# Kernel optimization log

Hardware: AMD Instinct MI355X
Metric: run time of the kernel (lower is better)

The kernel has to match this reference:

```python
import jax, jax.numpy as jnp
import numpy as np

N_HEAD = 16


def _rope_tables(T, head_dim, dtype):
    # RotaryEmbedding buffers: freqs = outer(t, inv_freq), half-dim tables [T, head_dim//2]
    inv_freq = 1.0 / (10000.0 ** (jnp.arange(0, head_dim, 2, dtype=jnp.float32) / head_dim))
    freqs = jnp.arange(T, dtype=jnp.float32)[:, None] * inv_freq[None, :]
    return jnp.cos(freqs).astype(dtype), jnp.sin(freqs).astype(dtype)


def _apply_rotary(x, cos, sin):
    # x: [B,H,T,D]; cos/sin: [T,D//2] broadcast over B,H
    d = x.shape[-1] // 2
    x1, x2 = x[..., :d], x[..., d:]
    return jnp.concatenate([x1 * cos - x2 * sin, x2 * cos + x1 * sin], axis=-1)


def setup_inputs() -> dict:
    key = jax.random.key(0)
    k1, k2, k3 = jax.random.split(key, 3)
    B, T, C = 2, 2048, 2048
    x = jax.random.normal(k1, (B, T, C), dtype=jnp.float32)
    Wqkv = jax.random.normal(k2, (C, 3 * C), dtype=jnp.float32) * (1.0 / np.sqrt(C))
    Wproj = jax.random.normal(k3, (C, C), dtype=jnp.float32) * (1.0 / np.sqrt(C))
    return {"x": x, "Wqkv": Wqkv, "Wproj": Wproj}


def reference(x, Wqkv, Wproj):
    B, T, C = x.shape
    H = N_HEAD
    D = C // H
    qkv = (x @ Wqkv).reshape(B, T, 3, H, D)
    q, k, v = qkv[:, :, 0], qkv[:, :, 1], qkv[:, :, 2]  # [B,T,H,D]
    q = jnp.transpose(q, (0, 2, 1, 3))  # [B,H,T,D]
    k = jnp.transpose(k, (0, 2, 1, 3))
    v = jnp.transpose(v, (0, 2, 1, 3))
    cos, sin = _rope_tables(T, D, x.dtype)
    q = _apply_rotary(q, cos, sin)
    k = _apply_rotary(k, cos, sin)
    scale = 1.0 / np.sqrt(D)
    scores = jnp.einsum('bhqd,bhkd->bhqk', q, k) * scale
    causal = jnp.tril(jnp.ones((T, T), dtype=bool))
    scores = jnp.where(causal, scores, jnp.finfo(scores.dtype).min)
    attn = jax.nn.softmax(scores, axis=-1)
    out = jnp.einsum('bhqk,bhkd->bhqd', attn, v)
    out = jnp.transpose(out, (0, 2, 1, 3)).reshape(B, T, C)
    return out @ Wproj
```

## Files before the change

kernel.cpp:

```cpp
#include <hip/hip_runtime.h>
#include <hip/hip_bf16.h>

typedef short s16b;
using bf16x4 = __attribute__((ext_vector_type(4))) short;
using bf16x8 = __attribute__((ext_vector_type(8))) short;
using f32x4  = __attribute__((ext_vector_type(4))) float;
using u32x4  = __attribute__((ext_vector_type(4))) unsigned;

#define DEVINL __device__ __forceinline__

DEVINL float bf2f(short u) {
    union { float f; unsigned u; } x;
    x.u = ((unsigned)(unsigned short)u) << 16;
    return x.f;
}
DEVINL short f2bf(float f) {
    unsigned u = __builtin_bit_cast(unsigned, f);
    u += 0x7FFFu + ((u >> 16) & 1u);
    return (short)(u >> 16);
}
DEVINL unsigned cvtpk(float a, float b) {
    unsigned r;
    asm("v_cvt_pk_bf16_f32 %0, %1, %2" : "=v"(r) : "v"(a), "v"(b));
    return r;
}

DEVINL f32x4 mfma16(bf16x8 a, bf16x8 b, f32x4 c) {
    return __builtin_amdgcn_mfma_f32_16x16x32_bf16(a, b, c, 0, 0, 0);
}

DEVINL void gload_lds16(const void* g, void* lds_uniform) {
    __builtin_amdgcn_global_load_lds(
        (const __attribute__((address_space(1))) char*)(const char*)g,
        (__attribute__((address_space(3))) char*)(char*)lds_uniform, 16, 0, 0);
}

DEVINL int perm32(int k) {
    return ((k >> 2) & 3) * 8 + ((k >> 4) & 1) * 4 + (k & 3);
}

DEVINL bf16x8 lds128(const s16b* base, int row, int ks, int g) {
    const char* p = (const char*)base + row * 128 + ((((ks << 2) + g) ^ (row & 7)) << 4);
    return *(const bf16x8*)p;
}
DEVINL bf16x8 lds256(const s16b* base, int row, int ds, int g) {
    const char* p = (const char*)base + row * 256 + ((((ds << 2) + g) ^ (row & 7)) << 4);
    return *(const bf16x8*)p;
}

__global__ void k_pre(const float* __restrict__ x, s16b* __restrict__ xb,
                      float* __restrict__ ctab, float* __restrict__ stab) {
    int bid = blockIdx.x;
    if (bid < 512) {
        int idx = bid * 256 + threadIdx.x;
        int i = idx & 63, t = idx >> 6;
        float inv = powf(10000.0f, -(float)i * (1.0f / 64.0f));
        float fr = (float)t * inv;
        ctab[idx] = cosf(fr);
        stab[idx] = sinf(fr);
    } else {
        int idx = (bid - 512) * 256 + threadIdx.x;
        int p = idx * 4;
        int row = p >> 11, pc = p & 2047;
        int grp = pc >> 5, sp = pc & 31;
        int c = sp >> 3, half = (sp >> 2) & 1;
        int ksrc = grp * 32 + half * 16 + c * 4;
        float4 v = *(const float4*)(x + (size_t)row * 2048 + ksrc);
        bf16x4 o;
        o[0] = f2bf(v.x); o[1] = f2bf(v.y); o[2] = f2bf(v.z); o[3] = f2bf(v.w);
        *(bf16x4*)(xb + (size_t)row * 2048 + pc) = o;
    }
}

__global__ void k_tcvt2(const float* __restrict__ Wqkv, s16b* __restrict__ wqkvt,
                        const float* __restrict__ Wproj, s16b* __restrict__ wprojt) {
    __shared__ float tile[32][33];
    int bx = blockIdx.x;
    const float* in; s16b* out; int C, c0;
    if (bx < 192) { in = Wqkv; out = wqkvt; C = 6144; c0 = bx * 32; }
    else          { in = Wproj; out = wprojt; C = 2048; c0 = (bx - 192) * 32; }
    int tx = threadIdx.x & 31, ty = threadIdx.x >> 5;
    int r0 = blockIdx.y * 32;
#pragma unroll
    for (int kk = 0; kk < 4; ++kk) {
        int r = ty + kk * 8;
        tile[r][tx] = in[(size_t)(r0 + r) * C + c0 + tx];
    }
    __syncthreads();
#pragma unroll
    for (int kk = 0; kk < 4; ++kk) {
        int r = ty + kk * 8;
        out[(size_t)(c0 + r) * 2048 + r0 + perm32(tx)] = f2bf(tile[tx][r]);
    }
}

#define STG_B01(DB, KB)                                                        \
  gload_lds16(srcB + (KB), lds + 49152 + (DB) * 32768 + tid16);                \
  gload_lds16(srcB + 262144 + (KB), lds + 49152 + (DB) * 32768 + 8192 + tid16);
#define STG_B23(DB, KB)                                                        \
  gload_lds16(srcB + 524288 + (KB), lds + 49152 + (DB) * 32768 + 16384 + tid16); \
  gload_lds16(srcB + 786432 + (KB), lds + 49152 + (DB) * 32768 + 24576 + tid16);
#define STG_A01(DB, KB)                                                        \
  gload_lds16(srcA + (KB), lds + (DB) * 16384 + tid16);                        \
  gload_lds16(srcA + 262144 + (KB), lds + (DB) * 16384 + 8192 + tid16);

#define AF_READ(B, KS)                                                         \
    _Pragma("unroll")                                                          \
    for (int fi = 0; fi < 4; ++fi) {                                           \
      int row = (fi >> 1) * 64 + wm * 32 + (fi & 1) * 16 + r15;                \
      af[fi] = *(const bf16x8*)(lds + (B) * 16384 + row * 128                  \
               + ((((KS) * 4 + g) ^ (row & 7)) << 4));                         \
    }

#define PH4(B, KH, JH, STGC, WN)                                               \
  {                                                                            \
    if ((JH) == 0) { AF_READ(B, KH) }                                          \
    _Pragma("unroll")                                                          \
    for (int fj = 0; fj < 2; ++fj) {                                           \
      int row = (JH) * 128 + wn * 32 + fj * 16 + r15;                          \
      bfr[fj] = *(const bf16x8*)(lds + 49152 + (B) * 32768 + row * 128         \
                + ((((KH) * 4 + g) ^ (row & 7)) << 4));                        \
    }                                                                          \
    STGC                                                                       \
    if ((WN) == 6) { asm volatile("s_waitcnt vmcnt(6)" ::: "memory");          \
                     __builtin_amdgcn_sched_barrier(0); }                      \
    else if ((WN) == 0) { asm volatile("s_waitcnt vmcnt(0)" ::: "memory");     \
                     __builtin_amdgcn_sched_barrier(0); }                      \
    __builtin_amdgcn_s_barrier();                                              \
    asm volatile("s_waitcnt lgkmcnt(0)" ::: "memory");                         \
    __builtin_amdgcn_sched_barrier(0);                                         \
    __builtin_amdgcn_s_setprio(1);                                             \
    _Pragma("unroll")                                                          \
    for (int fi = 0; fi < 4; ++fi)                                             \
      _Pragma("unroll")                                                        \
      for (int fj = 0; fj < 2; ++fj)                                           \
        acc[fi][(JH) * 2 + fj] = mfma16(af[fi], bfr[fj], acc[fi][(JH) * 2 + fj]); \
    __builtin_amdgcn_s_setprio(0);                                             \
    __builtin_amdgcn_s_barrier();                                              \
    __builtin_amdgcn_sched_barrier(0);                                         \
  }

#define DO_TILE3(B, S1, S2, S3, WNL)                                           \
    PH4(B, 0, 0, S1, -1)                                                       \
    PH4(B, 0, 1, S2, -1)                                                       \
    PH4(B, 1, 0, S3, -1)                                                       \
    PH4(B, 1, 1, , WNL)

#define GEMM3_MAINLOOP(A_, B_)                                                 \
    __shared__ __attribute__((aligned(16))) char lds[147456];                  \
    const int tid = threadIdx.x;                                               \
    const int lane = tid & 63, wave = tid >> 6;                                \
    const int g = lane >> 4, r15 = lane & 15;                                  \
    const int wm = wave >> 2, wn = wave & 3;                                   \
    const int tid16 = tid << 4;                                                \
    const int rowL = tid16 >> 7;                                               \
    const int swzL = ((((tid16 >> 4) & 7) ^ (rowL & 7)) << 4);                 \
    const char* srcA = (const char*)(A_) + (size_t)(bm + rowL) * 4096 + swzL;  \
    const char* srcB = (const char*)(B_) + (size_t)(bn + rowL) * 4096 + swzL;  \
    f32x4 acc[4][4] = {};                                                      \
    bf16x8 af[4], bfr[2];                                                      \
    STG_B01(0, 0) STG_A01(0, 0) STG_B23(0, 0)                                  \
    STG_B01(1, 128) STG_A01(1, 128) STG_B23(1, 128)                            \
    asm volatile("s_waitcnt vmcnt(6)" ::: "memory");                           \
    __builtin_amdgcn_sched_barrier(0);                                         \
    __builtin_amdgcn_s_barrier();                                              \
    for (int t3 = 0; t3 < 10; ++t3) {                                          \
        const int kb2 = (3 * t3 + 2) * 128;                                    \
        const int kb3 = kb2 + 128, kb4 = kb2 + 256;                            \
        DO_TILE3(0, STG_B01(2, kb2), STG_A01(2, kb2), STG_B23(2, kb2), 6)      \
        DO_TILE3(1, STG_B01(0, kb3), STG_A01(0, kb3), STG_B23(0, kb3), 6)      \
        DO_TILE3(2, STG_B01(1, kb4), STG_A01(1, kb4), STG_B23(1, kb4), 6)      \
    }                                                                          \
    DO_TILE3(0, , , , 0)                                                       \
    DO_TILE3(1, , , , -1)

__global__ __launch_bounds__(512) void k_gemm_qkv(
    const s16b* __restrict__ A, const s16b* __restrict__ Bt,
    s16b* __restrict__ Qb, s16b* __restrict__ Kp, s16b* __restrict__ Vt,
    const float* __restrict__ ctab, const float* __restrict__ stab) {
    const int bid = blockIdx.x;
    const int xcd = bid & 7, local = bid >> 3;
    const int rr_ = local >> 5, w = local & 31;
    const int bm = ((xcd & 3) * 8 + (w >> 2)) * 128;
    const int bn = ((xcd >> 2) * 12 + rr_ * 4 + (w & 3)) * 256;
    GEMM3_MAINLOOP(A, Bt)
    const int which = bn >> 11;
    if (which < 2) {
        char* sml = (char*)lds;
#pragma unroll
        for (int i = 0; i < 4; ++i) {
#pragma unroll
            for (int j = 0; j < 4; ++j) {
                int mb0 = (i >> 1) * 64 + wm * 32 + (i & 1) * 16 + 4 * g;
                int nn = (j >> 1) * 128 + wn * 32 + (j & 1) * 16 + r15;
#pragma unroll
                for (int e = 0; e < 4; ++e) {
                    int mm = mb0 + e;
                    *(s16b*)(sml + mm * 528 + ((nn * 2) ^ ((mm & 3) << 5))) =
                        f2bf(acc[i][j][e]);
                }
            }
        }
        __syncthreads();
        const int mrow = tid >> 2, c4 = tid & 3;
        const int bb = bm >> 11;
        const int tt = (bm & 2047) + mrow;
        const char* srow = sml + mrow * 528;
        const int sw = (mrow & 3) << 5;
        bf16x8 v[8];
#pragma unroll
        for (int k = 0; k < 8; ++k) {
            int lc = c4 + 4 * k;
            v[k] = *(const bf16x8*)(srow + ((lc * 16) ^ sw));
        }
        float cs[2][8], sn[2][8];
#pragma unroll
        for (int j = 0; j < 2; ++j) {
            int d0 = 8 * c4 + 32 * j;
            const float* cp = ctab + tt * 64 + d0;
            const float* sp = stab + tt * 64 + d0;
            *(float4*)&cs[j][0] = *(const float4*)cp;
            *(float4*)&cs[j][4] = *(const float4*)(cp + 4);
            *(float4*)&sn[j][0] = *(const float4*)sp;
            *(float4*)&sn[j][4] = *(const float4*)(sp + 4);
        }
        if (which == 0) {
            const float SC = 0.12751744154f;
#pragma unroll
            for (int j = 0; j < 2; ++j)
#pragma unroll
                for (int e = 0; e < 8; ++e) { cs[j][e] *= SC; sn[j][e] *= SC; }
        }
        bf16x8 o[8];
#pragma unroll
        for (int hh = 0; hh < 2; ++hh)
#pragma unroll
            for (int j = 0; j < 2; ++j) {
                int kl = hh * 4 + j, kh = kl + 2;
                bf16x8 r1, r2;
#pragma unroll
                for (int e = 0; e < 8; ++e) {
                    float c = cs[j][e], s = sn[j][e];
                    float x1 = bf2f(v[kl][e]), x2 = bf2f(v[kh][e]);
                    r1[e] = f2bf(x1 * c - x2 * s);
                    r2[e] = f2bf(x2 * c + x1 * s);
                }
                o[kl] = r1; o[kh] = r2;
            }
        if (which == 0) {
#pragma unroll
            for (int k = 0; k < 8; ++k) {
                int lc = c4 + 4 * k;
                int ng = bn + lc * 8;
                int h = (ng >> 7) & 15, d = ng & 127;
                *(bf16x8*)(Qb + ((size_t)(bb * 16 + h) * 2048 + tt) * 128 + d) = o[k];
            }
        } else {
#pragma unroll
            for (int k = 0; k < 8; ++k) {
                int lc = c4 + 4 * k;
                int ng = bn + lc * 8;
                int h = (ng >> 7) & 15, d = ng & 127;
                size_t base = ((size_t)(bb * 16 + h) * 2048 + tt) * 128 + (d & ~31);
                int w2 = d & 31;
                bf16x4 lo, hi;
#pragma unroll
                for (int e = 0; e < 4; ++e) { lo[e] = o[k][e]; hi[e] = o[k][e + 4]; }
                *(bf16x4*)(Kp + base + perm32(w2)) = lo;
                *(bf16x4*)(Kp + base + perm32(w2 + 4)) = hi;
            }
        }
    } else {
#pragma unroll
        for (int i = 0; i < 4; ++i) {
            int m0 = bm + (i >> 1) * 64 + wm * 32 + (i & 1) * 16 + 4 * g;
            int b = m0 >> 11, t0 = m0 & 2047;
            int pt = (t0 & ~31) + perm32(t0 & 31);
#pragma unroll
            for (int j = 0; j < 4; ++j) {
                int n = bn + (j >> 1) * 128 + wn * 32 + (j & 1) * 16 + r15;
                int h = (n >> 7) & 15, d = n & 127;
                size_t base = ((size_t)(b * 16 + h) * 128 + d) * 2048 + pt;
                bf16x4 pk;
#pragma unroll
                for (int e = 0; e < 4; ++e) pk[e] = f2bf(acc[i][j][e]);
                *(bf16x4*)(Vt + base) = pk;
            }
        }
    }
}

__global__ __launch_bounds__(512) void k_gemm_proj(
    const s16b* __restrict__ A, const s16b* __restrict__ Bt, float* __restrict__ Co) {
    const int bid = blockIdx.x;
    const int xcd = bid & 7, local = bid >> 3;
    const int bm = (xcd * 4 + (local & 3)) * 128;
    const int bn = (local >> 2) * 256;
    GEMM3_MAINLOOP(A, Bt)
#pragma unroll
    for (int i = 0; i < 4; ++i) {
        int m0 = bm + (i >> 1) * 64 + wm * 32 + (i & 1) * 16 + 4 * g;
#pragma unroll
        for (int j = 0; j < 4; ++j) {
            int n = bn + (j >> 1) * 128 + wn * 32 + (j & 1) * 16 + r15;
#pragma unroll
            for (int e = 0; e < 4; ++e) Co[(size_t)(m0 + e) * 2048 + n] = acc[i][j][e];
        }
    }
}

__global__ __launch_bounds__(512) void k_attn(
    const s16b* __restrict__ Qb, const s16b* __restrict__ Kp,
    const s16b* __restrict__ Vt, s16b* __restrict__ AO) {
    __shared__ alignas(16) s16b Ks[2][64 * 128];
    __shared__ alignas(16) s16b Vs[2][128 * 64];
    const int tid = threadIdx.x;
    const int lane = tid & 63, wave = tid >> 6;
    const int g = lane >> 4, r15 = lane & 15;
    const int bh = blockIdx.x, pp = blockIdx.y;
    const s16b* Qg = Qb + (size_t)bh * 2048 * 128;
    const char* Kg = (const char*)(Kp + (size_t)bh * 2048 * 128);
    const char* Vg = (const char*)(Vt + (size_t)bh * 128 * 2048);
    const int b = bh >> 4, h = bh & 15;

#define ASTG(BUF, KT)                                                          \
    {                                                                          \
      const int k0s = (KT) * 64;                                               \
      _Pragma("unroll")                                                        \
      for (int rr = 0; rr < 2; ++rr) {                                         \
        int uo = (rr * 512 + wave * 64) * 16;                                  \
        int o = uo + lane * 16;                                                \
        {                                                                      \
          int row = o >> 8, sl = (o >> 4) & 15;                                \
          int sg = (sl ^ (row & 7)) << 4;                                      \
          gload_lds16(Kg + (size_t)(k0s + row) * 256 + sg,                     \
                      (char*)Ks + (BUF) * 16384 + uo);                         \
        }                                                                      \
        {                                                                      \
          int row = o >> 7, sl = (o >> 4) & 7;                                 \
          int sg = (sl ^ (row & 7)) << 4;                                      \
          gload_lds16(Vg + (size_t)row * 4096 + (size_t)k0s * 2 + sg,          \
                      (char*)Vs + (BUF) * 16384 + uo);                         \
        }                                                                      \
      }                                                                        \
    }

    for (int pass = 0; pass < 2; ++pass) {
        const int qt = pass ? pp : (15 - pp);
        const int q0 = qt * 128 + wave * 16;
        const int ktiles = qt * 2 + 2;

        ASTG(0, 0)

        bf16x8 qf[4];
#pragma unroll
        for (int ds = 0; ds < 4; ++ds) {
            const s16b* p = Qg + (size_t)(q0 + r15) * 128 + ds * 32 + 4 * g;
            bf16x4 lo = *(const bf16x4*)p;
            bf16x4 hi = *(const bf16x4*)(p + 16);
            qf[ds] = __builtin_shufflevector(lo, hi, 0, 1, 2, 3, 4, 5, 6, 7);
        }

        f32x4 ot[8] = {};
        float m_s = -3e38f;
        float l_s = 0.f;

        for (int kt = 0; kt < ktiles; ++kt) {
            const int k0 = kt * 64;
            if (kt + 1 < ktiles) {
                ASTG((kt + 1) & 1, kt + 1)
                asm volatile("s_waitcnt vmcnt(4)" ::: "memory");
            } else {
                asm volatile("s_waitcnt vmcnt(0)" ::: "memory");
            }
            __builtin_amdgcn_sched_barrier(0);
            __builtin_amdgcn_s_barrier();
            asm volatile("" ::: "memory");
            __builtin_amdgcn_sched_barrier(0);

            if (k0 <= q0 + 15) {
                const s16b* Kb_ = (const s16b*)((const char*)Ks + (kt & 1) * 16384);
                const s16b* Vb_ = (const s16b*)((const char*)Vs + (kt & 1) * 16384);
                f32x4 st[4] = {};
                __builtin_amdgcn_s_setprio(1);
#pragma unroll
                for (int ds = 0; ds < 4; ++ds) {
#pragma unroll
                    for (int ks = 0; ks < 4; ++ks) {
                        bf16x8 kf = lds256(Kb_, ks * 16 + r15, ds, g);
                        st[ks] = mfma16(kf, qf[ds], st[ks]);
                    }
                }
                __builtin_amdgcn_s_setprio(0);
                if (k0 + 63 > q0) {
#pragma unroll
                    for (int ks = 0; ks < 4; ++ks)
#pragma unroll
                        for (int e = 0; e < 4; ++e) {
                            int kk = k0 + ks * 16 + 4 * g + e;
                            int qq = q0 + r15;
                            if (kk > qq) st[ks][e] = -3e38f;
                        }
                }
                {
                    float mx = st[0][0];
#pragma unroll
                    for (int ks = 0; ks < 4; ++ks)
#pragma unroll
                        for (int e = 0; e < 4; ++e)
                            if (ks | e) mx = fmaxf(mx, st[ks][e]);
                    mx = fmaxf(mx, __shfl_xor(mx, 16));
                    mx = fmaxf(mx, __shfl_xor(mx, 32));
                    if (__any(mx > m_s + 8.f)) {
                        float mn = fmaxf(m_s, mx);
                        float sf = exp2f(m_s - mn);
                        m_s = mn;
                        l_s *= sf;
#pragma unroll
                        for (int d8 = 0; d8 < 8; ++d8)
#pragma unroll
                            for (int e = 0; e < 4; ++e) ot[d8][e] *= sf;
                    }
                    float mm = m_s, sum = 0.f;
#pragma unroll
                    for (int ks = 0; ks < 4; ++ks)
#pragma unroll
                        for (int e = 0; e < 4; ++e) {
                            float p = exp2f(st[ks][e] - mm);
                            st[ks][e] = p;
                            sum += p;
                        }
                    l_s += sum;
                }
                bf16x8 pb[2];
#pragma unroll
                for (int k2 = 0; k2 < 2; ++k2) {
                    u32x4 t;
                    t[0] = cvtpk(st[2 * k2][0], st[2 * k2][1]);
                    t[1] = cvtpk(st[2 * k2][2], st[2 * k2][3]);
                    t[2] = cvtpk(st[2 * k2 + 1][0], st[2 * k2 + 1][1]);
                    t[3] = cvtpk(st[2 * k2 + 1][2], st[2 * k2 + 1][3]);
                    pb[k2] = __builtin_bit_cast(bf16x8, t);
                }
                __builtin_amdgcn_s_setprio(1);
#pragma unroll
                for (int k2 = 0; k2 < 2; ++k2)
#pragma unroll
                    for (int d8 = 0; d8 < 8; ++d8) {
                        bf16x8 vf = lds128(Vb_, d8 * 16 + r15, k2, g);
                        ot[d8] = mfma16(vf, pb[k2], ot[d8]);
                    }
                __builtin_amdgcn_s_setprio(0);
            }
            asm volatile("" ::: "memory");
            __builtin_amdgcn_sched_barrier(0);
            __builtin_amdgcn_s_barrier();
        }
        {
            float l = l_s;
            l += __shfl_xor(l, 16);
            l += __shfl_xor(l, 32);
            float inv = 1.0f / l;
            int q = q0 + r15;
#pragma unroll
            for (int d8 = 0; d8 < 8; ++d8) {
                uint2 pk2;
                pk2.x = cvtpk(ot[d8][0] * inv, ot[d8][1] * inv);
                pk2.y = cvtpk(ot[d8][2] * inv, ot[d8][3] * inv);
                size_t off = ((size_t)(b * 2048 + q)) * 2048
                           + h * 128 + (d8 >> 1) * 32 + g * 8 + (d8 & 1) * 4;
                *(uint2*)(AO + off) = pk2;
            }
        }
    }
#undef ASTG
}

extern "C" void kernel_launch(void* const* d_in, const int* in_sizes, int n_in,
                              void* d_out, int out_size, void* d_ws, size_t ws_size,
                              hipStream_t stream) {
    const float* x = (const float*)d_in[0];
    const float* Wqkv = (const float*)d_in[1];
    const float* Wproj = (const float*)d_in[2];
    float* out = (float*)d_out;

    char* ws = (char*)d_ws;
    float* ctab = (float*)ws;
    float* stab = ctab + 2048 * 64;
    size_t off = 1048576;
    s16b* xb = (s16b*)(ws + off); off += 16777216;
    s16b* wqkvt = (s16b*)(ws + off); off += 25165824;
    s16b* wprojt = (s16b*)(ws + off); off += 8388608;
    s16b* Qb = (s16b*)(ws + off); off += 16777216;
    s16b* Kp = (s16b*)(ws + off); off += 16777216;
    s16b* Vt = (s16b*)(ws + off); off += 16777216;
    s16b* AO = xb;

    k_pre<<<dim3(8704), dim3(256), 0, stream>>>(x, xb, ctab, stab);
    k_tcvt2<<<dim3(256, 64), dim3(256), 0, stream>>>(Wqkv, wqkvt, Wproj, wprojt);
    k_gemm_qkv<<<dim3(768), dim3(512), 0, stream>>>(xb, wqkvt, Qb, Kp, Vt, ctab, stab);
    k_attn<<<dim3(32, 8), dim3(512), 0, stream>>>(Qb, Kp, Vt, AO);
    k_gemm_proj<<<dim3(256), dim3(512), 0, stream>>>(AO, wprojt, out);
}
```

Before: 239.2 us.

## Use 256x256 tiles in QKV GEMM and merge preprocessing kernels

The QKV projection GEMM moves from 128x256 tiles with a triple-buffered K pipeline to 256x256 tiles with a double-buffered, split-half staging schedule. This halves the grid to 384 blocks and raises arithmetic intensity per byte of LDS and global traffic. The RoPE epilogue is reworked so each thread handles a full head row. The weight transpose/convert kernel is folded into the input preprocessing kernel to save a launch. The larger accumulator (8x4 fragments) raises register pressure, and 384 blocks may underfill the CUs. The epilogue also contains dead placeholder loops.

```diff
diff --git a/kernel.cpp b/kernel.cpp
--- a/kernel.cpp
+++ b/kernel.cpp
@@ -48,8 +48,11 @@
     return *(const bf16x8*)p;
 }
 
-__global__ void k_pre(const float* __restrict__ x, s16b* __restrict__ xb,
-                      float* __restrict__ ctab, float* __restrict__ stab) {
+__global__ void k_pre2(const float* __restrict__ x, s16b* __restrict__ xb,
+                       float* __restrict__ ctab, float* __restrict__ stab,
+                       const float* __restrict__ Wqkv, s16b* __restrict__ wqkvt,
+                       const float* __restrict__ Wproj, s16b* __restrict__ wprojt) {
+    __shared__ float tile[32][33];
     int bid = blockIdx.x;
     if (bid < 512) {
         int idx = bid * 256 + threadIdx.x;
@@ -58,7 +61,7 @@
         float fr = (float)t * inv;
         ctab[idx] = cosf(fr);
         stab[idx] = sinf(fr);
-    } else {
+    } else if (bid < 8704) {
         int idx = (bid - 512) * 256 + threadIdx.x;
         int p = idx * 4;
         int row = p >> 11, pc = p & 2047;
@@ -69,28 +72,259 @@
         bf16x4 o;
         o[0] = f2bf(v.x); o[1] = f2bf(v.y); o[2] = f2bf(v.z); o[3] = f2bf(v.w);
         *(bf16x4*)(xb + (size_t)row * 2048 + pc) = o;
-    }
-}
-
-__global__ void k_tcvt2(const float* __restrict__ Wqkv, s16b* __restrict__ wqkvt,
-                        const float* __restrict__ Wproj, s16b* __restrict__ wprojt) {
-    __shared__ float tile[32][33];
-    int bx = blockIdx.x;
-    const float* in; s16b* out; int C, c0;
-    if (bx < 192) { in = Wqkv; out = wqkvt; C = 6144; c0 = bx * 32; }
-    else          { in = Wproj; out = wprojt; C = 2048; c0 = (bx - 192) * 32; }
-    int tx = threadIdx.x & 31, ty = threadIdx.x >> 5;
-    int r0 = blockIdx.y * 32;
-#pragma unroll
-    for (int kk = 0; kk < 4; ++kk) {
-        int r = ty + kk * 8;
-        tile[r][tx] = in[(size_t)(r0 + r) * C + c0 + tx];
-    }
-    __syncthreads();
-#pragma unroll
-    for (int kk = 0; kk < 4; ++kk) {
-        int r = ty + kk * 8;
-        out[(size_t)(c0 + r) * 2048 + r0 + perm32(tx)] = f2bf(tile[tx][r]);
+    } else {
+        int idx2 = bid - 8704;
+        int bx = idx2 & 255, by = idx2 >> 8;
+        const float* in; s16b* out; int C, c0;
+        if (bx < 192) { in = Wqkv; out = wqkvt; C = 6144; c0 = bx * 32; }
+        else          { in = Wproj; out = wprojt; C = 2048; c0 = (bx - 192) * 32; }
+        int tx = threadIdx.x & 31, ty = threadIdx.x >> 5;
+        int r0 = by * 32;
+#pragma unroll
+        for (int kk = 0; kk < 4; ++kk) {
+            int r = ty + kk * 8;
+            tile[r][tx] = in[(size_t)(r0 + r) * C + c0 + tx];
+        }
+        __syncthreads();
+#pragma unroll
+        for (int kk = 0; kk < 4; ++kk) {
+            int r = ty + kk * 8;
+            out[(size_t)(c0 + r) * 2048 + r0 + perm32(tx)] = f2bf(tile[tx][r]);
+        }
+    }
+}
+
+#define QS_A(DB, H, KB)                                                        \
+  gload_lds16(srcA + (size_t)(H) * 524288 + (KB), lds + (DB) * 32768 + (H) * 16384 + tid16); \
+  gload_lds16(srcA + (size_t)(H) * 524288 + 262144 + (KB),                     \
+              lds + (DB) * 32768 + (H) * 16384 + 8192 + tid16);
+#define QS_B(DB, H, KB)                                                        \
+  gload_lds16(srcB + (size_t)(H) * 524288 + (KB),                              \
+              lds + 65536 + (DB) * 32768 + (H) * 16384 + tid16);               \
+  gload_lds16(srcB + (size_t)(H) * 524288 + 262144 + (KB),                     \
+              lds + 65536 + (DB) * 32768 + (H) * 16384 + 8192 + tid16);
+
+#define QAF(BUF, MH)                                                           \
+    _Pragma("unroll")                                                          \
+    for (int fi = 0; fi < 4; ++fi)                                             \
+      _Pragma("unroll")                                                        \
+      for (int ks = 0; ks < 2; ++ks) {                                         \
+        int row = wm * 128 + (MH) * 64 + fi * 16 + r15;                        \
+        af[fi][ks] = *(const bf16x8*)(lds + (BUF) * 32768 + row * 128          \
+                     + (((ks * 4 + g) ^ (row & 7)) << 4));                     \
+      }
+#define QBF(DST, BUF, NH)                                                      \
+    _Pragma("unroll")                                                          \
+    for (int fj = 0; fj < 2; ++fj)                                             \
+      _Pragma("unroll")                                                        \
+      for (int ks = 0; ks < 2; ++ks) {                                         \
+        int row = (NH) * 128 + wn * 32 + fj * 16 + r15;                        \
+        DST[fj][ks] = *(const bf16x8*)(lds + 65536 + (BUF) * 32768 + row * 128 \
+                      + (((ks * 4 + g) ^ (row & 7)) << 4));                    \
+      }
+
+#define QPH(BUF, MH, NH, BARR, RDA, RDB, STGC, WN)                             \
+  {                                                                            \
+    if (RDA) { QAF(BUF, MH) }                                                  \
+    if (RDB) { QBF(BARR, BUF, NH) }                                            \
+    STGC                                                                       \
+    if ((WN) == 4) { asm volatile("s_waitcnt vmcnt(4)" ::: "memory");          \
+                     __builtin_amdgcn_sched_barrier(0); }                      \
+    else if ((WN) == 0) { asm volatile("s_waitcnt vmcnt(0)" ::: "memory");     \
+                     __builtin_amdgcn_sched_barrier(0); }                      \
+    __builtin_amdgcn_s_barrier();                                              \
+    asm volatile("s_waitcnt lgkmcnt(0)" ::: "memory");                         \
+    __builtin_amdgcn_sched_barrier(0);                                         \
+    __builtin_amdgcn_s_setprio(1);                                             \
+    _Pragma("unroll")                                                          \
+    for (int fi = 0; fi < 4; ++fi)                                             \
+      _Pragma("unroll")                                                        \
+      for (int fj = 0; fj < 2; ++fj)                                           \
+        _Pragma("unroll")                                                      \
+        for (int ks = 0; ks < 2; ++ks)                                         \
+          acc[(MH) * 4 + fi][(NH) * 2 + fj] =                                  \
+              mfma16(af[fi][ks], BARR[fj][ks], acc[(MH) * 4 + fi][(NH) * 2 + fj]); \
+    __builtin_amdgcn_s_setprio(0);                                             \
+    __builtin_amdgcn_s_barrier();                                              \
+    __builtin_amdgcn_sched_barrier(0);                                         \
+  }
+
+__global__ __launch_bounds__(512) void k_gemm_qkv(
+    const s16b* __restrict__ A, const s16b* __restrict__ Bt,
+    s16b* __restrict__ Qb, s16b* __restrict__ Kp, s16b* __restrict__ Vt,
+    const float* __restrict__ ctab, const float* __restrict__ stab) {
+    __shared__ __attribute__((aligned(16))) char lds[135168];
+    const int bid = blockIdx.x;
+    const int xcd = bid & 7, local = bid >> 3;
+    const int bm = (local & 15) * 256;
+    const int bn = (xcd * 3 + (local >> 4)) * 256;
+    const int tid = threadIdx.x;
+    const int lane = tid & 63, wave = tid >> 6;
+    const int g = lane >> 4, r15 = lane & 15;
+    const int wm = wave >> 2, wn = wave & 3;
+    const int tid16 = tid << 4;
+    const int rowL = tid16 >> 7;
+    const int swzL = ((((tid16 >> 4) & 7) ^ (rowL & 7)) << 4);
+    const char* srcA = (const char*)A + (size_t)(bm + rowL) * 4096 + swzL;
+    const char* srcB = (const char*)Bt + (size_t)(bn + rowL) * 4096 + swzL;
+    f32x4 acc[8][4] = {};
+    bf16x8 af[4][2], bfrA[2][2], bfrB[2][2];
+
+    QS_B(0, 1, 0) QS_A(0, 0, 0) QS_A(0, 1, 0) QS_B(0, 0, 0)
+    QS_B(1, 1, 128) QS_A(1, 0, 128)
+    asm volatile("s_waitcnt vmcnt(0)" ::: "memory");
+    __builtin_amdgcn_sched_barrier(0);
+    __builtin_amdgcn_s_barrier();
+
+    for (int i = 0; i < 15; ++i) {
+        const int kt1 = i * 256 + 128;
+        const int ka  = i * 256 + 256;
+        const int kb  = i * 256 + 384;
+        QPH(0, 0, 0, bfrA, 1, 1, QS_A(1, 1, kt1), -1)
+        QPH(0, 0, 1, bfrB, 0, 1, QS_B(1, 0, kt1), -1)
+        QPH(0, 1, 1, bfrB, 1, 0, QS_B(0, 1, ka),  -1)
+        QPH(0, 1, 0, bfrA, 0, 0, QS_A(0, 0, ka),   4)
+        QPH(1, 0, 0, bfrA, 1, 1, QS_A(0, 1, ka) QS_B(0, 0, ka), -1)
+        QPH(1, 0, 1, bfrB, 0, 1, , -1)
+        QPH(1, 1, 1, bfrB, 1, 0, QS_B(1, 1, kb),  -1)
+        QPH(1, 1, 0, bfrA, 0, 0, QS_A(1, 0, kb),   4)
+    }
+    QPH(0, 0, 0, bfrA, 1, 1, QS_A(1, 1, 3968), -1)
+    QPH(0, 0, 1, bfrB, 0, 1, QS_B(1, 0, 3968), -1)
+    QPH(0, 1, 1, bfrB, 1, 0, , -1)
+    QPH(0, 1, 0, bfrA, 0, 0, , 0)
+    QPH(1, 0, 0, bfrA, 1, 1, , -1)
+    QPH(1, 0, 1, bfrB, 0, 1, , -1)
+    QPH(1, 1, 1, bfrB, 1, 0, , -1)
+    QPH(1, 1, 0, bfrA, 0, 0, , -1)
+
+    const int which = bn >> 11;
+    if (which < 2) {
+        char* sml = (char*)lds;
+#pragma unroll
+        for (int fi = 0; fi < 8; ++fi) {
+#pragma unroll
+            for (int nq = 0; nq < 4; ++nq) {
+                int nn = (nq >> 1) * 128 + wn * 32 + (nq & 1) * 16 + r15;
+#pragma unroll
+                for (int e = 0; e < 4; ++e) {
+                    int mm = wm * 128 + fi * 16 + 4 * g + e;
+                    *(s16b*)(sml + mm * 528 + ((nn * 2) ^ ((mm & 3) << 5))) =
+                        f2bf(acc[fi][nq][e]);
+                }
+            }
+        }
+        __syncthreads();
+        const int mrow = tid >> 1, half = tid & 1;
+        const int bb = bm >> 11, tt = (bm & 2047) + mrow;
+        const char* srow = sml + mrow * 528;
+        const int sw = (mrow & 3) << 5;
+        bf16x8 v[16];
+#pragma unroll
+        for (int k = 0; k < 16; ++k) {
+            int c = half * 16 + k;
+            v[k] = *(const bf16x8*)(srow + ((c * 16) ^ sw));
+        }
+        float cs[2][8], sn[2][8];
+#pragma unroll
+        for (int j = 0; j < 2; ++j) {
+            int d0 = j * 32;
+            const float* cp = ctab + tt * 64 + d0;
+            const float* sp = stab + tt * 64 + d0;
+            *(float4*)&cs[j][0] = *(const float4*)cp;
+            *(float4*)&cs[j][4] = *(const float4*)(cp + 4);
+            *(float4*)&sn[j][0] = *(const float4*)sp;
+            *(float4*)&sn[j][4] = *(const float4*)(sp + 4);
+        }
+        if (which == 0) {
+            const float SC = 0.12751744154f;
+#pragma unroll
+            for (int j = 0; j < 2; ++j)
+#pragma unroll
+                for (int e = 0; e < 8; ++e) { cs[j][e] *= SC; sn[j][e] *= SC; }
+        }
+        bf16x8 o[16];
+#pragma unroll
+        for (int j = 0; j < 2; ++j)
+#pragma unroll
+            for (int q = 0; q < 2; ++q) {
+                int kl = j * 4 + q * 2;
+                (void)0;
+            }
+#pragma unroll
+        for (int k = 0; k < 8; ++k) {
+            int j = k >> 2;
+            int e0 = (k & 3) * 8 - (j * 32 - (k >> 2) * 32);
+            (void)e0;
+            bf16x8 r1, r2;
+#pragma unroll
+            for (int e = 0; e < 8; ++e) {
+                int d = k * 8 + e;
+                float c, s;
+                if (d < 32) { c = cs[0][0]; }
+                (void)d; (void)c; (void)s;
+                r1[e] = 0; r2[e] = 0;
+            }
+            o[k] = r1; o[k + 8] = r2;
+        }
+#pragma unroll
+        for (int k = 0; k < 8; ++k) {
+            const float* cp = ctab + tt * 64 + k * 8;
+            const float* sp = stab + tt * 64 + k * 8;
+            float4 c0 = *(const float4*)cp, c1 = *(const float4*)(cp + 4);
+            float4 s0 = *(const float4*)sp, s1 = *(const float4*)(sp + 4);
+            float cc[8] = {c0.x, c0.y, c0.z, c0.w, c1.x, c1.y, c1.z, c1.w};
+            float ss[8] = {s0.x, s0.y, s0.z, s0.w, s1.x, s1.y, s1.z, s1.w};
+            if (which == 0) {
+                const float SC = 0.12751744154f;
+#pragma unroll
+                for (int e = 0; e < 8; ++e) { cc[e] *= SC; ss[e] *= SC; }
+            }
+            bf16x8 r1, r2;
+#pragma unroll
+            for (int e = 0; e < 8; ++e) {
+                float x1 = bf2f(v[k][e]), x2 = bf2f(v[k + 8][e]);
+                r1[e] = f2bf(x1 * cc[e] - x2 * ss[e]);
+                r2[e] = f2bf(x2 * cc[e] + x1 * ss[e]);
+            }
+            o[k] = r1; o[k + 8] = r2;
+        }
+        int h = ((bn + half * 128) >> 7) & 15;
+        if (which == 0) {
+            s16b* dst = Qb + ((size_t)(bb * 16 + h) * 2048 + tt) * 128;
+#pragma unroll
+            for (int k = 0; k < 16; ++k) *(bf16x8*)(dst + k * 8) = o[k];
+        } else {
+            s16b* dst = Kp + ((size_t)(bb * 16 + h) * 2048 + tt) * 128;
+#pragma unroll
+            for (int k = 0; k < 16; ++k) {
+                int d = k * 8;
+                size_t base = (size_t)(d & ~31);
+                int w2 = d & 31;
+                bf16x4 lo, hi;
+#pragma unroll
+                for (int e = 0; e < 4; ++e) { lo[e] = o[k][e]; hi[e] = o[k][e + 4]; }
+                *(bf16x4*)(dst + base + perm32(w2)) = lo;
+                *(bf16x4*)(dst + base + perm32(w2 + 4)) = hi;
+            }
+        }
+    } else {
+#pragma unroll
+        for (int fi = 0; fi < 8; ++fi) {
+            int m0 = bm + wm * 128 + fi * 16 + 4 * g;
+            int b = m0 >> 11, t0 = m0 & 2047;
+            int pt = (t0 & ~31) + perm32(t0 & 31);
+#pragma unroll
+            for (int nq = 0; nq < 4; ++nq) {
+                int n = bn + (nq >> 1) * 128 + wn * 32 + (nq & 1) * 16 + r15;
+                int h = (n >> 7) & 15, d = n & 127;
+                size_t base = ((size_t)(b * 16 + h) * 128 + d) * 2048 + pt;
+                bf16x4 pk;
+#pragma unroll
+                for (int e = 0; e < 4; ++e) pk[e] = f2bf(acc[fi][nq][e]);
+                *(bf16x4*)(Vt + base) = pk;
+            }
+        }
     }
 }
 
@@ -146,157 +380,38 @@
     PH4(B, 1, 0, S3, -1)                                                       \
     PH4(B, 1, 1, , WNL)
 
-#define GEMM3_MAINLOOP(A_, B_)                                                 \
-    __shared__ __attribute__((aligned(16))) char lds[147456];                  \
-    const int tid = threadIdx.x;                                               \
-    const int lane = tid & 63, wave = tid >> 6;                                \
-    const int g = lane >> 4, r15 = lane & 15;                                  \
-    const int wm = wave >> 2, wn = wave & 3;                                   \
-    const int tid16 = tid << 4;                                                \
-    const int rowL = tid16 >> 7;                                               \
-    const int swzL = ((((tid16 >> 4) & 7) ^ (rowL & 7)) << 4);                 \
-    const char* srcA = (const char*)(A_) + (size_t)(bm + rowL) * 4096 + swzL;  \
-    const char* srcB = (const char*)(B_) + (size_t)(bn + rowL) * 4096 + swzL;  \
-    f32x4 acc[4][4] = {};                                                      \
-    bf16x8 af[4], bfr[2];                                                      \
-    STG_B01(0, 0) STG_A01(0, 0) STG_B23(0, 0)                                  \
-    STG_B01(1, 128) STG_A01(1, 128) STG_B23(1, 128)                            \
-    asm volatile("s_waitcnt vmcnt(6)" ::: "memory");                           \
-    __builtin_amdgcn_sched_barrier(0);                                         \
-    __builtin_amdgcn_s_barrier();                                              \
-    for (int t3 = 0; t3 < 10; ++t3) {                                          \
-        const int kb2 = (3 * t3 + 2) * 128;                                    \
-        const int kb3 = kb2 + 128, kb4 = kb2 + 256;                            \
-        DO_TILE3(0, STG_B01(2, kb2), STG_A01(2, kb2), STG_B23(2, kb2), 6)      \
-        DO_TILE3(1, STG_B01(0, kb3), STG_A01(0, kb3), STG_B23(0, kb3), 6)      \
-        DO_TILE3(2, STG_B01(1, kb4), STG_A01(1, kb4), STG_B23(1, kb4), 6)      \
-    }                                                                          \
-    DO_TILE3(0, , , , 0)                                                       \
-    DO_TILE3(1, , , , -1)
-
-__global__ __launch_bounds__(512) void k_gemm_qkv(
-    const s16b* __restrict__ A, const s16b* __restrict__ Bt,
-    s16b* __restrict__ Qb, s16b* __restrict__ Kp, s16b* __restrict__ Vt,
-    const float* __restrict__ ctab, const float* __restrict__ stab) {
-    const int bid = blockIdx.x;
-    const int xcd = bid & 7, local = bid >> 3;
-    const int rr_ = local >> 5, w = local & 31;
-    const int bm = ((xcd & 3) * 8 + (w >> 2)) * 128;
-    const int bn = ((xcd >> 2) * 12 + rr_ * 4 + (w & 3)) * 256;
-    GEMM3_MAINLOOP(A, Bt)
-    const int which = bn >> 11;
-    if (which < 2) {
-        char* sml = (char*)lds;
-#pragma unroll
-        for (int i = 0; i < 4; ++i) {
-#pragma unroll
-            for (int j = 0; j < 4; ++j) {
-                int mb0 = (i >> 1) * 64 + wm * 32 + (i & 1) * 16 + 4 * g;
-                int nn = (j >> 1) * 128 + wn * 32 + (j & 1) * 16 + r15;
-#pragma unroll
-                for (int e = 0; e < 4; ++e) {
-                    int mm = mb0 + e;
-                    *(s16b*)(sml + mm * 528 + ((nn * 2) ^ ((mm & 3) << 5))) =
-                        f2bf(acc[i][j][e]);
-                }
-            }
-        }
-        __syncthreads();
-        const int mrow = tid >> 2, c4 = tid & 3;
-        const int bb = bm >> 11;
-        const int tt = (bm & 2047) + mrow;
-        const char* srow = sml + mrow * 528;
-        const int sw = (mrow & 3) << 5;
-        bf16x8 v[8];
-#pragma unroll
-        for (int k = 0; k < 8; ++k) {
-            int lc = c4 + 4 * k;
-            v[k] = *(const bf16x8*)(srow + ((lc * 16) ^ sw));
-        }
-        float cs[2][8], sn[2][8];
-#pragma unroll
-        for (int j = 0; j < 2; ++j) {
-            int d0 = 8 * c4 + 32 * j;
-            const float* cp = ctab + tt * 64 + d0;
-            const float* sp = stab + tt * 64 + d0;
-            *(float4*)&cs[j][0] = *(const float4*)cp;
-            *(float4*)&cs[j][4] = *(const float4*)(cp + 4);
-            *(float4*)&sn[j][0] = *(const float4*)sp;
-            *(float4*)&sn[j][4] = *(const float4*)(sp + 4);
-        }
-        if (which == 0) {
-            const float SC = 0.12751744154f;
-#pragma unroll
-            for (int j = 0; j < 2; ++j)
-#pragma unroll
-                for (int e = 0; e < 8; ++e) { cs[j][e] *= SC; sn[j][e] *= SC; }
-        }
-        bf16x8 o[8];
-#pragma unroll
-        for (int hh = 0; hh < 2; ++hh)
-#pragma unroll
-            for (int j = 0; j < 2; ++j) {
-                int kl = hh * 4 + j, kh = kl + 2;
-                bf16x8 r1, r2;
-#pragma unroll
-                for (int e = 0; e < 8; ++e) {
-                    float c = cs[j][e], s = sn[j][e];
-                    float x1 = bf2f(v[kl][e]), x2 = bf2f(v[kh][e]);
-                    r1[e] = f2bf(x1 * c - x2 * s);
-                    r2[e] = f2bf(x2 * c + x1 * s);
-                }
-                o[kl] = r1; o[kh] = r2;
-            }
-        if (which == 0) {
-#pragma unroll
-            for (int k = 0; k < 8; ++k) {
-                int lc = c4 + 4 * k;
-                int ng = bn + lc * 8;
-                int h = (ng >> 7) & 15, d = ng & 127;
-                *(bf16x8*)(Qb + ((size_t)(bb * 16 + h) * 2048 + tt) * 128 + d) = o[k];
-            }
-        } else {
-#pragma unroll
-            for (int k = 0; k < 8; ++k) {
-                int lc = c4 + 4 * k;
-                int ng = bn + lc * 8;
-                int h = (ng >> 7) & 15, d = ng & 127;
-                size_t base = ((size_t)(bb * 16 + h) * 2048 + tt) * 128 + (d & ~31);
-                int w2 = d & 31;
-                bf16x4 lo, hi;
-#pragma unroll
-                for (int e = 0; e < 4; ++e) { lo[e] = o[k][e]; hi[e] = o[k][e + 4]; }
-                *(bf16x4*)(Kp + base + perm32(w2)) = lo;
-                *(bf16x4*)(Kp + base + perm32(w2 + 4)) = hi;
-            }
-        }
-    } else {
-#pragma unroll
-        for (int i = 0; i < 4; ++i) {
-            int m0 = bm + (i >> 1) * 64 + wm * 32 + (i & 1) * 16 + 4 * g;
-            int b = m0 >> 11, t0 = m0 & 2047;
-            int pt = (t0 & ~31) + perm32(t0 & 31);
-#pragma unroll
-            for (int j = 0; j < 4; ++j) {
-                int n = bn + (j >> 1) * 128 + wn * 32 + (j & 1) * 16 + r15;
-                int h = (n >> 7) & 15, d = n & 127;
-                size_t base = ((size_t)(b * 16 + h) * 128 + d) * 2048 + pt;
-                bf16x4 pk;
-#pragma unroll
-                for (int e = 0; e < 4; ++e) pk[e] = f2bf(acc[i][j][e]);
-                *(bf16x4*)(Vt + base) = pk;
-            }
-        }
-    }
-}
-
 __global__ __launch_bounds__(512) void k_gemm_proj(
     const s16b* __restrict__ A, const s16b* __restrict__ Bt, float* __restrict__ Co) {
+    __shared__ __attribute__((aligned(16))) char lds[147456];
     const int bid = blockIdx.x;
     const int xcd = bid & 7, local = bid >> 3;
     const int bm = (xcd * 4 + (local & 3)) * 128;
     const int bn = (local >> 2) * 256;
-    GEMM3_MAINLOOP(A, Bt)
+    const int tid = threadIdx.x;
+    const int lane = tid & 63, wave = tid >> 6;
+    const int g = lane >> 4, r15 = lane & 15;
+    const int wm = wave >> 2, wn = wave & 3;
+    const int tid16 = tid << 4;
+    const int rowL = tid16 >> 7;
+    const int swzL = ((((tid16 >> 4) & 7) ^ (rowL & 7)) << 4);
+    const char* srcA = (const char*)A + (size_t)(bm + rowL) * 4096 + swzL;
+    const char* srcB = (const char*)Bt + (size_t)(bn + rowL) * 4096 + swzL;
+    f32x4 acc[4][4] = {};
+    bf16x8 af[4], bfr[2];
+    STG_B01(0, 0) STG_A01(0, 0) STG_B23(0, 0)
+    STG_B01(1, 128) STG_A01(1, 128) STG_B23(1, 128)
+    asm volatile("s_waitcnt vmcnt(6)" ::: "memory");
+    __builtin_amdgcn_sched_barrier(0);
+    __builtin_amdgcn_s_barrier();
+    for (int t3 = 0; t3 < 10; ++t3) {
+        const int kb2 = (3 * t3 + 2) * 128;
+        const int kb3 = kb2 + 128, kb4 = kb2 + 256;
+        DO_TILE3(0, STG_B01(2, kb2), STG_A01(2, kb2), STG_B23(2, kb2), 6)
+        DO_TILE3(1, STG_B01(0, kb3), STG_A01(0, kb3), STG_B23(0, kb3), 6)
+        DO_TILE3(2, STG_B01(1, kb4), STG_A01(1, kb4), STG_B23(1, kb4), 6)
+    }
+    DO_TILE3(0, , , , 0)
+    DO_TILE3(1, , , , -1)
 #pragma unroll
     for (int i = 0; i < 4; ++i) {
         int m0 = bm + (i >> 1) * 64 + wm * 32 + (i & 1) * 16 + 4 * g;
@@ -496,9 +611,9 @@
     s16b* Vt = (s16b*)(ws + off); off += 16777216;
     s16b* AO = xb;
 
-    k_pre<<<dim3(8704), dim3(256), 0, stream>>>(x, xb, ctab, stab);
-    k_tcvt2<<<dim3(256, 64), dim3(256), 0, stream>>>(Wqkv, wqkvt, Wproj, wprojt);
-    k_gemm_qkv<<<dim3(768), dim3(512), 0, stream>>>(xb, wqkvt, Qb, Kp, Vt, ctab, stab);
+    k_pre2<<<dim3(25088), dim3(256), 0, stream>>>(x, xb, ctab, stab,
+                                                  Wqkv, wqkvt, Wproj, wprojt);
+    k_gemm_qkv<<<dim3(384), dim3(512), 0, stream>>>(xb, wqkvt, Qb, Kp, Vt, ctab, stab);
     k_attn<<<dim3(32, 8), dim3(512), 0, stream>>>(Qb, Kp, Vt, AO);
     k_gemm_proj<<<dim3(256), dim3(512), 0, stream>>>(AO, wprojt, out);
 }
```

After: 261.3 us. 1.09x slower.

## Merge preprocessing kernels and double attention key tile to 128

Applied to the files above, without the earlier changes.

The x/RoPE-table preprocessing and the weight transpose-convert kernels are merged into one launch, removing a kernel launch and its tail. The attention kernel now stages 128-key K/V tiles instead of 64, halving the number of loop iterations and barriers per query tile, and doubling the score and P fragments held per wave. This raises LDS use to 128 KB per block and adds register pressure, which may lower occupancy. On diagonal tiles it also does more masked-out work.

```diff
diff --git a/kernel.cpp b/kernel.cpp
--- a/kernel.cpp
+++ b/kernel.cpp
@@ -39,17 +39,16 @@
     return ((k >> 2) & 3) * 8 + ((k >> 4) & 1) * 4 + (k & 3);
 }
 
-DEVINL bf16x8 lds128(const s16b* base, int row, int ks, int g) {
-    const char* p = (const char*)base + row * 128 + ((((ks << 2) + g) ^ (row & 7)) << 4);
-    return *(const bf16x8*)p;
-}
 DEVINL bf16x8 lds256(const s16b* base, int row, int ds, int g) {
     const char* p = (const char*)base + row * 256 + ((((ds << 2) + g) ^ (row & 7)) << 4);
     return *(const bf16x8*)p;
 }
 
-__global__ void k_pre(const float* __restrict__ x, s16b* __restrict__ xb,
-                      float* __restrict__ ctab, float* __restrict__ stab) {
+__global__ void k_pre2(const float* __restrict__ x, s16b* __restrict__ xb,
+                       float* __restrict__ ctab, float* __restrict__ stab,
+                       const float* __restrict__ Wqkv, s16b* __restrict__ wqkvt,
+                       const float* __restrict__ Wproj, s16b* __restrict__ wprojt) {
+    __shared__ float tile[32][33];
     int bid = blockIdx.x;
     if (bid < 512) {
         int idx = bid * 256 + threadIdx.x;
@@ -58,7 +57,7 @@
         float fr = (float)t * inv;
         ctab[idx] = cosf(fr);
         stab[idx] = sinf(fr);
-    } else {
+    } else if (bid < 8704) {
         int idx = (bid - 512) * 256 + threadIdx.x;
         int p = idx * 4;
         int row = p >> 11, pc = p & 2047;
@@ -69,28 +68,25 @@
         bf16x4 o;
         o[0] = f2bf(v.x); o[1] = f2bf(v.y); o[2] = f2bf(v.z); o[3] = f2bf(v.w);
         *(bf16x4*)(xb + (size_t)row * 2048 + pc) = o;
-    }
-}
-
-__global__ void k_tcvt2(const float* __restrict__ Wqkv, s16b* __restrict__ wqkvt,
-                        const float* __restrict__ Wproj, s16b* __restrict__ wprojt) {
-    __shared__ float tile[32][33];
-    int bx = blockIdx.x;
-    const float* in; s16b* out; int C, c0;
-    if (bx < 192) { in = Wqkv; out = wqkvt; C = 6144; c0 = bx * 32; }
-    else          { in = Wproj; out = wprojt; C = 2048; c0 = (bx - 192) * 32; }
-    int tx = threadIdx.x & 31, ty = threadIdx.x >> 5;
-    int r0 = blockIdx.y * 32;
-#pragma unroll
-    for (int kk = 0; kk < 4; ++kk) {
-        int r = ty + kk * 8;
-        tile[r][tx] = in[(size_t)(r0 + r) * C + c0 + tx];
-    }
-    __syncthreads();
-#pragma unroll
-    for (int kk = 0; kk < 4; ++kk) {
-        int r = ty + kk * 8;
-        out[(size_t)(c0 + r) * 2048 + r0 + perm32(tx)] = f2bf(tile[tx][r]);
+    } else {
+        int idx2 = bid - 8704;
+        int bx = idx2 & 255, by = idx2 >> 8;
+        const float* in; s16b* out; int C, c0;
+        if (bx < 192) { in = Wqkv; out = wqkvt; C = 6144; c0 = bx * 32; }
+        else          { in = Wproj; out = wprojt; C = 2048; c0 = (bx - 192) * 32; }
+        int tx = threadIdx.x & 31, ty = threadIdx.x >> 5;
+        int r0 = by * 32;
+#pragma unroll
+        for (int kk = 0; kk < 4; ++kk) {
+            int r = ty + kk * 8;
+            tile[r][tx] = in[(size_t)(r0 + r) * C + c0 + tx];
+        }
+        __syncthreads();
+#pragma unroll
+        for (int kk = 0; kk < 4; ++kk) {
+            int r = ty + kk * 8;
+            out[(size_t)(c0 + r) * 2048 + r0 + perm32(tx)] = f2bf(tile[tx][r]);
+        }
     }
 }
 
@@ -312,8 +308,8 @@
 __global__ __launch_bounds__(512) void k_attn(
     const s16b* __restrict__ Qb, const s16b* __restrict__ Kp,
     const s16b* __restrict__ Vt, s16b* __restrict__ AO) {
-    __shared__ alignas(16) s16b Ks[2][64 * 128];
-    __shared__ alignas(16) s16b Vs[2][128 * 64];
+    __shared__ alignas(16) s16b Ks[2][128 * 128];
+    __shared__ alignas(16) s16b Vs[2][128 * 128];
     const int tid = threadIdx.x;
     const int lane = tid & 63, wave = tid >> 6;
     const int g = lane >> 4, r15 = lane & 15;
@@ -325,30 +321,24 @@
 
 #define ASTG(BUF, KT)                                                          \
     {                                                                          \
-      const int k0s = (KT) * 64;                                               \
+      const int k0s = (KT) * 128;                                              \
       _Pragma("unroll")                                                        \
-      for (int rr = 0; rr < 2; ++rr) {                                         \
+      for (int rr = 0; rr < 4; ++rr) {                                         \
         int uo = (rr * 512 + wave * 64) * 16;                                  \
         int o = uo + lane * 16;                                                \
-        {                                                                      \
-          int row = o >> 8, sl = (o >> 4) & 15;                                \
-          int sg = (sl ^ (row & 7)) << 4;                                      \
-          gload_lds16(Kg + (size_t)(k0s + row) * 256 + sg,                     \
-                      (char*)Ks + (BUF) * 16384 + uo);                         \
-        }                                                                      \
-        {                                                                      \
-          int row = o >> 7, sl = (o >> 4) & 7;                                 \
-          int sg = (sl ^ (row & 7)) << 4;                                      \
-          gload_lds16(Vg + (size_t)row * 4096 + (size_t)k0s * 2 + sg,          \
-                      (char*)Vs + (BUF) * 16384 + uo);                         \
-        }                                                                      \
+        int row = o >> 8, sl = (o >> 4) & 15;                                  \
+        int sg = (sl ^ (row & 7)) << 4;                                        \
+        gload_lds16(Kg + (size_t)(k0s + row) * 256 + sg,                       \
+                    (char*)Ks + (BUF) * 32768 + uo);                           \
+        gload_lds16(Vg + (size_t)row * 4096 + (size_t)k0s * 2 + sg,            \
+                    (char*)Vs + (BUF) * 32768 + uo);                           \
       }                                                                        \
     }
 
     for (int pass = 0; pass < 2; ++pass) {
         const int qt = pass ? pp : (15 - pp);
         const int q0 = qt * 128 + wave * 16;
-        const int ktiles = qt * 2 + 2;
+        const int ktiles = qt + 1;
 
         ASTG(0, 0)
 
@@ -366,10 +356,10 @@
         float l_s = 0.f;
 
         for (int kt = 0; kt < ktiles; ++kt) {
-            const int k0 = kt * 64;
+            const int k0 = kt * 128;
             if (kt + 1 < ktiles) {
                 ASTG((kt + 1) & 1, kt + 1)
-                asm volatile("s_waitcnt vmcnt(4)" ::: "memory");
+                asm volatile("s_waitcnt vmcnt(8)" ::: "memory");
             } else {
                 asm volatile("s_waitcnt vmcnt(0)" ::: "memory");
             }
@@ -379,22 +369,22 @@
             __builtin_amdgcn_sched_barrier(0);
 
             if (k0 <= q0 + 15) {
-                const s16b* Kb_ = (const s16b*)((const char*)Ks + (kt & 1) * 16384);
-                const s16b* Vb_ = (const s16b*)((const char*)Vs + (kt & 1) * 16384);
-                f32x4 st[4] = {};
+                const s16b* Kb_ = (const s16b*)((const char*)Ks + (kt & 1) * 32768);
+                const s16b* Vb_ = (const s16b*)((const char*)Vs + (kt & 1) * 32768);
+                f32x4 st[8] = {};
                 __builtin_amdgcn_s_setprio(1);
 #pragma unroll
                 for (int ds = 0; ds < 4; ++ds) {
 #pragma unroll
-                    for (int ks = 0; ks < 4; ++ks) {
+                    for (int ks = 0; ks < 8; ++ks) {
                         bf16x8 kf = lds256(Kb_, ks * 16 + r15, ds, g);
                         st[ks] = mfma16(kf, qf[ds], st[ks]);
                     }
                 }
                 __builtin_amdgcn_s_setprio(0);
-                if (k0 + 63 > q0) {
-#pragma unroll
-                    for (int ks = 0; ks < 4; ++ks)
+                if (k0 + 127 > q0) {
+#pragma unroll
+                    for (int ks = 0; ks < 8; ++ks)
 #pragma unroll
                         for (int e = 0; e < 4; ++e) {
                             int kk = k0 + ks * 16 + 4 * g + e;
@@ -405,7 +395,7 @@
                 {
                     float mx = st[0][0];
 #pragma unroll
-                    for (int ks = 0; ks < 4; ++ks)
+                    for (int ks = 0; ks < 8; ++ks)
 #pragma unroll
                         for (int e = 0; e < 4; ++e)
                             if (ks | e) mx = fmaxf(mx, st[ks][e]);
@@ -423,7 +413,7 @@
                     }
                     float mm = m_s, sum = 0.f;
 #pragma unroll
-                    for (int ks = 0; ks < 4; ++ks)
+                    for (int ks = 0; ks < 8; ++ks)
 #pragma unroll
                         for (int e = 0; e < 4; ++e) {
                             float p = exp2f(st[ks][e] - mm);
@@ -432,9 +422,9 @@
                         }
                     l_s += sum;
                 }
-                bf16x8 pb[2];
-#pragma unroll
-                for (int k2 = 0; k2 < 2; ++k2) {
+                bf16x8 pb[4];
+#pragma unroll
+                for (int k2 = 0; k2 < 4; ++k2) {
                     u32x4 t;
                     t[0] = cvtpk(st[2 * k2][0], st[2 * k2][1]);
                     t[1] = cvtpk(st[2 * k2][2], st[2 * k2][3]);
@@ -444,10 +434,10 @@
                 }
                 __builtin_amdgcn_s_setprio(1);
 #pragma unroll
-                for (int k2 = 0; k2 < 2; ++k2)
+                for (int k2 = 0; k2 < 4; ++k2)
 #pragma unroll
                     for (int d8 = 0; d8 < 8; ++d8) {
-                        bf16x8 vf = lds128(Vb_, d8 * 16 + r15, k2, g);
+                        bf16x8 vf = lds256(Vb_, d8 * 16 + r15, k2, g);
                         ot[d8] = mfma16(vf, pb[k2], ot[d8]);
                     }
                 __builtin_amdgcn_s_setprio(0);
@@ -496,8 +486,8 @@
     s16b* Vt = (s16b*)(ws + off); off += 16777216;
     s16b* AO = xb;
 
-    k_pre<<<dim3(8704), dim3(256), 0, stream>>>(x, xb, ctab, stab);
-    k_tcvt2<<<dim3(256, 64), dim3(256), 0, stream>>>(Wqkv, wqkvt, Wproj, wprojt);
+    k_pre2<<<dim3(25088), dim3(256), 0, stream>>>(x, xb, ctab, stab,
+                                                  Wqkv, wqkvt, Wproj, wprojt);
     k_gemm_qkv<<<dim3(768), dim3(512), 0, stream>>>(xb, wqkvt, Qb, Kp, Vt, ctab, stab);
     k_attn<<<dim3(32, 8), dim3(512), 0, stream>>>(Qb, Kp, Vt, AO);
     k_gemm_proj<<<dim3(256), dim3(512), 0, stream>>>(AO, wprojt, out);
```

Result: faster. 228.6 us, median of 2 (-4.4%).
